# Kernel tuning notes

Measured on AMD Instinct MI355X. Metric: run time of the kernel, lower is better.

Reference implementation:

```python
import jax, jax.numpy as jnp
import numpy as np

NUM_FREQ = 10
HIDDEN = 256
ENC_DIM = 2 * 2 * NUM_FREQ  # input_dim * 2 * num_frequencies = 40
OUT_DIM = 3


def setup_inputs() -> dict:
    key = jax.random.key(0)
    ks = jax.random.split(key, 8)
    B, N = 4, 262144
    x = jax.random.uniform(ks[0], (B, N, 2), dtype=jnp.float32)
    # layer 0: enc_dim -> hidden
    W_in = jax.random.normal(ks[1], (ENC_DIM, HIDDEN), dtype=jnp.float32) * (1.0 / np.sqrt(ENC_DIM))
    b_in = jnp.zeros((HIDDEN,), dtype=jnp.float32)
    # layers 1..6: hidden -> hidden (6 of them)
    W_hid = jax.random.normal(ks[2], (6, HIDDEN, HIDDEN), dtype=jnp.float32) * (1.0 / np.sqrt(HIDDEN))
    b_hid = jnp.zeros((6, HIDDEN), dtype=jnp.float32)
    # layer 7: hidden -> out
    W_out = jax.random.normal(ks[3], (HIDDEN, OUT_DIM), dtype=jnp.float32) * (1.0 / np.sqrt(HIDDEN))
    b_out = jnp.zeros((OUT_DIM,), dtype=jnp.float32)
    return {"x": x, "W_in": W_in, "b_in": b_in, "W_hid": W_hid,
            "b_hid": b_hid, "W_out": W_out, "b_out": b_out}


def _pos_encode(x):
    # x: (B, N, 2) -> (B, N, 40). Matches torch: cat([sin, cos], -1) over freq axis then flatten.
    freq = 2.0 ** jnp.arange(NUM_FREQ, dtype=jnp.float32)  # (10,)
    xe = x[..., :, None] * freq  # (B, N, 2, 10)
    enc = jnp.concatenate([jnp.sin(xe), jnp.cos(xe)], axis=-1)  # (B, N, 2, 20)
    return enc.reshape(x.shape[0], x.shape[1], -1)  # (B, N, 40)


def reference(x, W_in, b_in, W_hid, b_hid, W_out, b_out):
    h = _pos_encode(x)
    h = jax.nn.relu(h @ W_in + b_in)
    for i in range(W_hid.shape[0]):  # 6 hidden layers, fixed small loop
        h = jax.nn.relu(h @ W_hid[i] + b_hid[i])
    out = jnp.tanh(h @ W_out + b_out) / 100.0
    return out
```

## Files before the change

kernel.cpp:

```cpp
#include <hip/hip_runtime.h>
#include <stdint.h>

#define THREADS 256
#define NBLOCKS 8192
#define BR      128

#define NG_STRIDE 204800
#define WS_WOUT   819200
#define WS_TOTAL  (WS_WOUT + 16384)

typedef short bf16x8 __attribute__((ext_vector_type(8)));
typedef float f32x16 __attribute__((ext_vector_type(16)));
typedef float f32x4v __attribute__((ext_vector_type(4)));

__device__ __forceinline__ unsigned short f2bf(float f) {
    union { float f; unsigned int u; } v; v.f = f;
    unsigned int u = v.u;
    u += 0x7fffu + ((u >> 16) & 1u);
    return (unsigned short)(u >> 16);
}
__device__ __forceinline__ unsigned int cvt_pk_bf16(float lo, float hi) {
    unsigned int d;
    asm("v_cvt_pk_bf16_f32 %0, %1, %2" : "=v"(d) : "v"(lo), "v"(hi));
    return d;
}

__global__ void prep_kernel(const float* __restrict__ W_in,
                            const float* __restrict__ W_hid,
                            const float* __restrict__ W_out,
                            unsigned char* __restrict__ ws) {
    int id = blockIdx.x * 256 + threadIdx.x;
    if (id < 16384) {
        int n = id & 255, k = id >> 8;
        int ng = n >> 6, ft = (n >> 5) & 1, ln = n & 31;
        int kk = k >> 4, hi = (k >> 3) & 1, e = k & 7;
        float v = (k < 40) ? W_in[k * 256 + n] : 0.f;
        *(unsigned short*)(ws + ng * NG_STRIDE + (kk * 2 + ft) * 1024
                           + (hi * 32 + ln) * 16 + e * 2) = f2bf(v);
    } else if (id < 16384 + 393216) {
        int e2 = id - 16384;
        int l = e2 >> 16, r = e2 & 65535;
        int k = r >> 8, n = r & 255;
        int c = k >> 6, kk = (k >> 4) & 3, hi = (k >> 3) & 1, e = k & 7;
        int ng = n >> 6, ft = (n >> 5) & 1, ln = n & 31;
        float v = W_hid[l * 65536 + k * 256 + n];
        *(unsigned short*)(ws + ng * NG_STRIDE + 8192 + l * 32768
                           + ((c * 4 + kk) * 2 + ft) * 1024
                           + (hi * 32 + ln) * 16 + e * 2) = f2bf(v);
    } else if (id < 16384 + 393216 + 8192) {
        int e3 = id - 16384 - 393216;
        int n = e3 >> 8, k = e3 & 255;
        int kk = k >> 4, hi = (k >> 3) & 1, e = k & 7;
        float v = (n < 3) ? W_out[k * 3 + n] : 0.f;
        *(unsigned short*)(ws + WS_WOUT + kk * 1024
                           + (hi * 32 + n) * 16 + e * 2) = f2bf(v);
    }
}

template <int NC>
__device__ __forceinline__ void layer_pass(const unsigned char* __restrict__ wl,
                                           const float* __restrict__ bp,
                                           unsigned char* actL, f32x16 (&acc)[2][4],
                                           int nblk, int l31,
                                           int hi, int hi16, int swz) {
    #pragma unroll
    for (int tn = 0; tn < 2; ++tn) {
        #pragma unroll
        for (int g4 = 0; g4 < 4; ++g4) {
            f32x4v bv = *(const f32x4v*)(bp + nblk + tn * 32 + g4 * 8 + hi * 4);
            #pragma unroll
            for (int tr = 0; tr < 4; ++tr) {
                #pragma unroll
                for (int j = 0; j < 4; ++j)
                    acc[tn][tr][g4 * 4 + j] = bv[j];
            }
        }
    }

    int io[4];
    #pragma unroll
    for (int kk = 0; kk < 4; ++kk) io[kk] = (kk * 32 + hi16) ^ swz;

    __builtin_amdgcn_s_setprio(1);
    #pragma unroll
    for (int c = 0; c < NC; ++c) {
        #pragma unroll
        for (int kk = 0; kk < 4; ++kk) {
            const unsigned char* fp = wl + (c * 4 + kk) * 2048;
            bf16x8 a0 = *(const bf16x8*)(fp);
            bf16x8 a1 = *(const bf16x8*)(fp + 1024);
            const int bo = c * 128 + io[kk];
            bf16x8 b0 = *(const bf16x8*)(actL + (      l31) * 512 + bo);
            bf16x8 b1 = *(const bf16x8*)(actL + (32  + l31) * 512 + bo);
            bf16x8 b2 = *(const bf16x8*)(actL + (64  + l31) * 512 + bo);
            bf16x8 b3 = *(const bf16x8*)(actL + (96  + l31) * 512 + bo);
            acc[0][0] = __builtin_amdgcn_mfma_f32_32x32x16_bf16(a0, b0, acc[0][0], 0, 0, 0);
            acc[1][0] = __builtin_amdgcn_mfma_f32_32x32x16_bf16(a1, b0, acc[1][0], 0, 0, 0);
            acc[0][1] = __builtin_amdgcn_mfma_f32_32x32x16_bf16(a0, b1, acc[0][1], 0, 0, 0);
            acc[1][1] = __builtin_amdgcn_mfma_f32_32x32x16_bf16(a1, b1, acc[1][1], 0, 0, 0);
            acc[0][2] = __builtin_amdgcn_mfma_f32_32x32x16_bf16(a0, b2, acc[0][2], 0, 0, 0);
            acc[1][2] = __builtin_amdgcn_mfma_f32_32x32x16_bf16(a1, b2, acc[1][2], 0, 0, 0);
            acc[0][3] = __builtin_amdgcn_mfma_f32_32x32x16_bf16(a0, b3, acc[0][3], 0, 0, 0);
            acc[1][3] = __builtin_amdgcn_mfma_f32_32x32x16_bf16(a1, b3, acc[1][3], 0, 0, 0);
        }
    }
    __builtin_amdgcn_s_setprio(0);

    __syncthreads();
    #pragma unroll
    for (int tr = 0; tr < 4; ++tr) {
        unsigned char* rowp = actL + (tr * 32 + l31) * 512;
        #pragma unroll
        for (int tn = 0; tn < 2; ++tn) {
            #pragma unroll
            for (int g4 = 0; g4 < 4; ++g4) {
                float v0 = fmaxf(acc[tn][tr][g4 * 4 + 0], 0.f);
                float v1 = fmaxf(acc[tn][tr][g4 * 4 + 1], 0.f);
                float v2 = fmaxf(acc[tn][tr][g4 * 4 + 2], 0.f);
                float v3 = fmaxf(acc[tn][tr][g4 * 4 + 3], 0.f);
                int n0b = (nblk + tn * 32 + g4 * 8 + hi * 4) * 2;
                uint2 u; u.x = cvt_pk_bf16(v0, v1); u.y = cvt_pk_bf16(v2, v3);
                *(uint2*)(rowp + (n0b ^ swz)) = u;
            }
        }
    }
    __syncthreads();
}

__global__ __launch_bounds__(THREADS, 2)
void nerf_main(const float* __restrict__ x,
               const float* __restrict__ b_in,
               const float* __restrict__ b_hid,
               const float* __restrict__ b_out,
               const unsigned char* __restrict__ ws,
               float* __restrict__ out) {
    __shared__ __align__(16) unsigned char actL[65536];

    const int tid  = threadIdx.x;
    const int lane = tid & 63;
    const int wv   = tid >> 6;
    const int l31  = lane & 31;
    const int hi   = lane >> 5;
    const int hi16 = hi << 4;
    const int swz  = (l31 & 7) << 4;
    const int nblk = wv * 64;
    const long gr0 = (long)blockIdx.x * BR;

    #pragma unroll
    for (int pass = 0; pass < 2; ++pass) {
        const int rr = (tid >> 2) + pass * 64;
        const int part = tid & 3;
        const int co = part >> 1, hf = part & 1;
        float xv = x[(gr0 + rr) * 2 + co];
        unsigned char* rowp = actL + rr * 512;
        const int rsw = (rr & 7) << 4;
        const int kb = co * 20 + hf * 10;
        float vv[10];
        #pragma unroll
        for (int f = 0; f < 10; ++f) {
            float ang = xv * (float)(1 << f);
            vv[f] = hf ? __cosf(ang) : __sinf(ang);
        }
        #pragma unroll
        for (int p = 0; p < 5; ++p) {
            unsigned int u = cvt_pk_bf16(vv[2 * p], vv[2 * p + 1]);
            int byte = (kb + 2 * p) * 2;
            *(unsigned int*)(rowp + (byte ^ rsw)) = u;
        }
        int z = 80 + part * 12;
        *(unsigned int*)(rowp + ((z    ) ^ rsw)) = 0u;
        *(unsigned int*)(rowp + ((z + 4) ^ rsw)) = 0u;
        *(unsigned int*)(rowp + ((z + 8) ^ rsw)) = 0u;
    }
    __syncthreads();

    f32x16 acc[2][4];
    const unsigned char* wstream = ws + wv * NG_STRIDE + lane * 16;

    layer_pass<1>(wstream, b_in, actL, acc, nblk, l31, hi, hi16, swz);
    wstream += 8192;

    #pragma unroll 1
    for (int l = 0; l < 6; ++l) {
        layer_pass<4>(wstream, b_hid + l * 256,
                      actL, acc, nblk, l31, hi, hi16, swz);
        wstream += 32768;
    }

    {
        f32x16 c0, c1;
        #pragma unroll
        for (int j = 0; j < 16; ++j) { c0[j] = 0.f; c1[j] = 0.f; }
        const unsigned char* wo   = ws + WS_WOUT + lane * 16;
        const unsigned char* arow = actL + (wv * 32 + l31) * 512;
        #pragma unroll
        for (int kk = 0; kk < 16; ++kk) {
            bf16x8 a = *(const bf16x8*)(wo + kk * 1024);
            bf16x8 b = *(const bf16x8*)(arow + (((kk * 32 + hi16)) ^ swz));
            if (kk & 1) c1 = __builtin_amdgcn_mfma_f32_32x32x16_bf16(a, b, c1, 0, 0, 0);
            else        c0 = __builtin_amdgcn_mfma_f32_32x32x16_bf16(a, b, c0, 0, 0, 0);
        }
        if (hi == 0) {
            long row = gr0 + wv * 32 + l31;
            float* op = out + row * 3;
            #pragma unroll
            for (int j = 0; j < 3; ++j)
                op[j] = tanhf(c0[j] + c1[j] + b_out[j]) * 0.01f;
        }
    }
}

extern "C" void kernel_launch(void* const* d_in, const int* in_sizes, int n_in,
                              void* d_out, int out_size, void* d_ws, size_t ws_size,
                              hipStream_t stream) {
    (void)in_sizes; (void)n_in; (void)out_size;
    const float* x     = (const float*)d_in[0];
    const float* W_in  = (const float*)d_in[1];
    const float* b_in  = (const float*)d_in[2];
    const float* W_hid = (const float*)d_in[3];
    const float* b_hid = (const float*)d_in[4];
    const float* W_out = (const float*)d_in[5];
    const float* b_out = (const float*)d_in[6];
    unsigned char* ws  = (unsigned char*)d_ws;
    float* out = (float*)d_out;

    if (ws_size < (size_t)WS_TOTAL) return;

    prep_kernel<<<1632, 256, 0, stream>>>(W_in, W_hid, W_out, ws);
    nerf_main<<<NBLOCKS, THREADS, 0, stream>>>(x, b_in, b_hid, b_out, ws, out);
}
```

Before: 731.2 us.

## Switch wave tiling to 2x2 to halve LDS activation reads per MFMA

Reassigns the four waves from a 1x4 split over output columns to a 2x2 split over rows and columns. Each wave now loads four weight fragments and two activation fragments per k-step instead of two and four. The weight pre-pack layout is changed to match. This reduces LDS read traffic but doubles the per-wave weight loads from global/L2.

```diff
diff --git a/kernel.cpp b/kernel.cpp
--- a/kernel.cpp
+++ b/kernel.cpp
@@ -5,9 +5,9 @@
 #define NBLOCKS 8192
 #define BR      128
 
-#define NG_STRIDE 204800
-#define WS_WOUT   819200
-#define WS_TOTAL  (WS_WOUT + 16384)
+#define NG2_STRIDE 409600
+#define WS_WOUT    819200
+#define WS_TOTAL   (WS_WOUT + 16384)
 
 typedef short bf16x8 __attribute__((ext_vector_type(8)));
 typedef float f32x16 __attribute__((ext_vector_type(16)));
@@ -32,27 +32,27 @@
     int id = blockIdx.x * 256 + threadIdx.x;
     if (id < 16384) {
         int n = id & 255, k = id >> 8;
-        int ng = n >> 6, ft = (n >> 5) & 1, ln = n & 31;
-        int kk = k >> 4, hi = (k >> 3) & 1, e = k & 7;
+        int h = n >> 7, ft = (n >> 5) & 3, ln = n & 31;
+        int ks = k >> 4, hi = (k >> 3) & 1, e = k & 7;
         float v = (k < 40) ? W_in[k * 256 + n] : 0.f;
-        *(unsigned short*)(ws + ng * NG_STRIDE + (kk * 2 + ft) * 1024
+        *(unsigned short*)(ws + h * NG2_STRIDE + (ks * 4 + ft) * 1024
                            + (hi * 32 + ln) * 16 + e * 2) = f2bf(v);
     } else if (id < 16384 + 393216) {
         int e2 = id - 16384;
         int l = e2 >> 16, r = e2 & 65535;
         int k = r >> 8, n = r & 255;
-        int c = k >> 6, kk = (k >> 4) & 3, hi = (k >> 3) & 1, e = k & 7;
-        int ng = n >> 6, ft = (n >> 5) & 1, ln = n & 31;
+        int ks = k >> 4, hi = (k >> 3) & 1, e = k & 7;
+        int h = n >> 7, ft = (n >> 5) & 3, ln = n & 31;
         float v = W_hid[l * 65536 + k * 256 + n];
-        *(unsigned short*)(ws + ng * NG_STRIDE + 8192 + l * 32768
-                           + ((c * 4 + kk) * 2 + ft) * 1024
+        *(unsigned short*)(ws + h * NG2_STRIDE + 16384 + l * 65536
+                           + (ks * 4 + ft) * 1024
                            + (hi * 32 + ln) * 16 + e * 2) = f2bf(v);
     } else if (id < 16384 + 393216 + 8192) {
         int e3 = id - 16384 - 393216;
         int n = e3 >> 8, k = e3 & 255;
-        int kk = k >> 4, hi = (k >> 3) & 1, e = k & 7;
+        int ks = k >> 4, hi = (k >> 3) & 1, e = k & 7;
         float v = (n < 3) ? W_out[k * 3 + n] : 0.f;
-        *(unsigned short*)(ws + WS_WOUT + kk * 1024
+        *(unsigned short*)(ws + WS_WOUT + ks * 1024
                            + (hi * 32 + n) * 16 + e * 2) = f2bf(v);
     }
 }
@@ -60,16 +60,16 @@
 template <int NC>
 __device__ __forceinline__ void layer_pass(const unsigned char* __restrict__ wl,
                                            const float* __restrict__ bp,
-                                           unsigned char* actL, f32x16 (&acc)[2][4],
-                                           int nblk, int l31,
+                                           unsigned char* actL, f32x16 (&acc)[4][2],
+                                           int wn, int wr, int l31,
                                            int hi, int hi16, int swz) {
     #pragma unroll
-    for (int tn = 0; tn < 2; ++tn) {
+    for (int tn = 0; tn < 4; ++tn) {
         #pragma unroll
         for (int g4 = 0; g4 < 4; ++g4) {
-            f32x4v bv = *(const f32x4v*)(bp + nblk + tn * 32 + g4 * 8 + hi * 4);
+            f32x4v bv = *(const f32x4v*)(bp + wn * 128 + tn * 32 + g4 * 8 + hi * 4);
             #pragma unroll
-            for (int tr = 0; tr < 4; ++tr) {
+            for (int tr = 0; tr < 2; ++tr) {
                 #pragma unroll
                 for (int j = 0; j < 4; ++j)
                     acc[tn][tr][g4 * 4 + j] = bv[j];
@@ -81,44 +81,44 @@
     #pragma unroll
     for (int kk = 0; kk < 4; ++kk) io[kk] = (kk * 32 + hi16) ^ swz;
 
+    const unsigned char* br0 = actL + (wr * 64      + l31) * 512;
+    const unsigned char* br1 = actL + (wr * 64 + 32 + l31) * 512;
+
     __builtin_amdgcn_s_setprio(1);
     #pragma unroll
-    for (int c = 0; c < NC; ++c) {
-        #pragma unroll
-        for (int kk = 0; kk < 4; ++kk) {
-            const unsigned char* fp = wl + (c * 4 + kk) * 2048;
-            bf16x8 a0 = *(const bf16x8*)(fp);
-            bf16x8 a1 = *(const bf16x8*)(fp + 1024);
-            const int bo = c * 128 + io[kk];
-            bf16x8 b0 = *(const bf16x8*)(actL + (      l31) * 512 + bo);
-            bf16x8 b1 = *(const bf16x8*)(actL + (32  + l31) * 512 + bo);
-            bf16x8 b2 = *(const bf16x8*)(actL + (64  + l31) * 512 + bo);
-            bf16x8 b3 = *(const bf16x8*)(actL + (96  + l31) * 512 + bo);
-            acc[0][0] = __builtin_amdgcn_mfma_f32_32x32x16_bf16(a0, b0, acc[0][0], 0, 0, 0);
-            acc[1][0] = __builtin_amdgcn_mfma_f32_32x32x16_bf16(a1, b0, acc[1][0], 0, 0, 0);
-            acc[0][1] = __builtin_amdgcn_mfma_f32_32x32x16_bf16(a0, b1, acc[0][1], 0, 0, 0);
-            acc[1][1] = __builtin_amdgcn_mfma_f32_32x32x16_bf16(a1, b1, acc[1][1], 0, 0, 0);
-            acc[0][2] = __builtin_amdgcn_mfma_f32_32x32x16_bf16(a0, b2, acc[0][2], 0, 0, 0);
-            acc[1][2] = __builtin_amdgcn_mfma_f32_32x32x16_bf16(a1, b2, acc[1][2], 0, 0, 0);
-            acc[0][3] = __builtin_amdgcn_mfma_f32_32x32x16_bf16(a0, b3, acc[0][3], 0, 0, 0);
-            acc[1][3] = __builtin_amdgcn_mfma_f32_32x32x16_bf16(a1, b3, acc[1][3], 0, 0, 0);
-        }
+    for (int ks = 0; ks < NC * 4; ++ks) {
+        const unsigned char* fp = wl + ks * 4096;
+        bf16x8 a0 = *(const bf16x8*)(fp);
+        bf16x8 a1 = *(const bf16x8*)(fp + 1024);
+        bf16x8 a2 = *(const bf16x8*)(fp + 2048);
+        bf16x8 a3 = *(const bf16x8*)(fp + 3072);
+        const int bo = (ks >> 2) * 128 + io[ks & 3];
+        bf16x8 b0 = *(const bf16x8*)(br0 + bo);
+        bf16x8 b1 = *(const bf16x8*)(br1 + bo);
+        acc[0][0] = __builtin_amdgcn_mfma_f32_32x32x16_bf16(a0, b0, acc[0][0], 0, 0, 0);
+        acc[1][0] = __builtin_amdgcn_mfma_f32_32x32x16_bf16(a1, b0, acc[1][0], 0, 0, 0);
+        acc[2][0] = __builtin_amdgcn_mfma_f32_32x32x16_bf16(a2, b0, acc[2][0], 0, 0, 0);
+        acc[3][0] = __builtin_amdgcn_mfma_f32_32x32x16_bf16(a3, b0, acc[3][0], 0, 0, 0);
+        acc[0][1] = __builtin_amdgcn_mfma_f32_32x32x16_bf16(a0, b1, acc[0][1], 0, 0, 0);
+        acc[1][1] = __builtin_amdgcn_mfma_f32_32x32x16_bf16(a1, b1, acc[1][1], 0, 0, 0);
+        acc[2][1] = __builtin_amdgcn_mfma_f32_32x32x16_bf16(a2, b1, acc[2][1], 0, 0, 0);
+        acc[3][1] = __builtin_amdgcn_mfma_f32_32x32x16_bf16(a3, b1, acc[3][1], 0, 0, 0);
     }
     __builtin_amdgcn_s_setprio(0);
 
     __syncthreads();
     #pragma unroll
-    for (int tr = 0; tr < 4; ++tr) {
-        unsigned char* rowp = actL + (tr * 32 + l31) * 512;
-        #pragma unroll
-        for (int tn = 0; tn < 2; ++tn) {
+    for (int tr = 0; tr < 2; ++tr) {
+        unsigned char* rowp = actL + (wr * 64 + tr * 32 + l31) * 512;
+        #pragma unroll
+        for (int tn = 0; tn < 4; ++tn) {
             #pragma unroll
             for (int g4 = 0; g4 < 4; ++g4) {
                 float v0 = fmaxf(acc[tn][tr][g4 * 4 + 0], 0.f);
                 float v1 = fmaxf(acc[tn][tr][g4 * 4 + 1], 0.f);
                 float v2 = fmaxf(acc[tn][tr][g4 * 4 + 2], 0.f);
                 float v3 = fmaxf(acc[tn][tr][g4 * 4 + 3], 0.f);
-                int n0b = (nblk + tn * 32 + g4 * 8 + hi * 4) * 2;
+                int n0b = (wn * 128 + tn * 32 + g4 * 8 + hi * 4) * 2;
                 uint2 u; u.x = cvt_pk_bf16(v0, v1); u.y = cvt_pk_bf16(v2, v3);
                 *(uint2*)(rowp + (n0b ^ swz)) = u;
             }
@@ -139,11 +139,12 @@
     const int tid  = threadIdx.x;
     const int lane = tid & 63;
     const int wv   = tid >> 6;
+    const int wn   = wv & 1;
+    const int wr   = wv >> 1;
     const int l31  = lane & 31;
     const int hi   = lane >> 5;
     const int hi16 = hi << 4;
     const int swz  = (l31 & 7) << 4;
-    const int nblk = wv * 64;
     const long gr0 = (long)blockIdx.x * BR;
 
     #pragma unroll
@@ -174,17 +175,17 @@
     }
     __syncthreads();
 
-    f32x16 acc[2][4];
-    const unsigned char* wstream = ws + wv * NG_STRIDE + lane * 16;
-
-    layer_pass<1>(wstream, b_in, actL, acc, nblk, l31, hi, hi16, swz);
-    wstream += 8192;
+    f32x16 acc[4][2];
+    const unsigned char* wstream = ws + wn * NG2_STRIDE + lane * 16;
+
+    layer_pass<1>(wstream, b_in, actL, acc, wn, wr, l31, hi, hi16, swz);
+    wstream += 16384;
 
     #pragma unroll 1
     for (int l = 0; l < 6; ++l) {
         layer_pass<4>(wstream, b_hid + l * 256,
-                      actL, acc, nblk, l31, hi, hi16, swz);
-        wstream += 32768;
+                      actL, acc, wn, wr, l31, hi, hi16, swz);
+        wstream += 65536;
     }
 
     {
```

Measured after the change: 776.6 us. 6.2% more time.
